# Optimization experiments

Measured on AMD Instinct MI355X. Metric: run time of the kernel, lower is better.

## Reference

```python
import jax, jax.numpy as jnp
import numpy as np

JITTER = 0.05  # posterior-covariance jitter (constructor arg `jitter`)
TWO_PI = 2.0 * np.pi


def _local_k(x1, x2, ls, std):
    # 1-D RBF kernel: x1 (A,), x2 (B,) -> (A, B)
    d2 = jnp.square(x1[:, None] - x2[None, :])
    return (std * std) * jnp.exp(-0.5 * d2 / (ls * ls))


def setup_inputs() -> dict:
    key = jax.random.key(0)
    ks = jax.random.split(key, 8)
    N, D, M = 3072, 4, 512
    X = jax.random.normal(ks[0], (N, D), dtype=jnp.float32)
    y = jax.random.normal(ks[1], (N, 1), dtype=jnp.float32)
    X_bar = jax.random.normal(ks[2], (M, D), dtype=jnp.float32)
    # learned parameters (moderate positive values so fp32 Choleskys are stable)
    local_gp_ls = 1.0 + 0.1 * jax.random.normal(ks[3], (D,), dtype=jnp.float32)
    local_gp_std = 0.5 + 0.05 * jax.random.normal(ks[4], (D,), dtype=jnp.float32)
    local_gp_noise_std = 0.3 * jnp.ones((D,), dtype=jnp.float32)
    local_ls = 0.3 + 0.5 * jax.random.uniform(ks[5], (M, D), dtype=jnp.float32)
    global_gp_std = jnp.array([0.7], dtype=jnp.float32)
    global_gp_noise_std = jnp.array([0.5], dtype=jnp.float32)
    return {
        "X": X, "y": y, "X_bar": X_bar,
        "local_gp_ls": local_gp_ls, "local_gp_std": local_gp_std,
        "local_gp_noise_std": local_gp_noise_std, "local_ls": local_ls,
        "global_gp_std": global_gp_std, "global_gp_noise_std": global_gp_noise_std,
    }


def reference(X, y, X_bar, local_gp_ls, local_gp_std, local_gp_noise_std,
              local_ls, global_gp_std, global_gp_noise_std):
    # NSGP.nlml() in training mode.
    N, D = X.shape
    M = X_bar.shape[0]
    dtype = X.dtype
    eyeM = jnp.eye(M, dtype=dtype)
    eyeN = jnp.eye(N, dtype=dtype)
    log_lbar = jnp.log(jnp.abs(local_ls))  # (M, D)

    def per_dim(xb, xd, ls, std, noise, loglb):
        # local GP over inducing points for one input dimension
        k = _local_k(xb, xb, ls, std) + (noise * noise) * eyeM  # (M, M)
        c = jnp.linalg.cholesky(k)
        alpha = jax.scipy.linalg.cho_solve((c, True), loglb[:, None])  # (M, 1)
        kstar = _local_k(xd, xb, ls, std)  # (N, M)
        l = jnp.exp(kstar @ alpha)[:, 0]   # (N,) predicted lengthscales
        kss = _local_k(xd, xd, ls, std)    # (N, N)
        v = jax.scipy.linalg.cho_solve((c, True), kstar.T)  # (M, N)
        kpost = kss - kstar @ v + JITTER * eyeN             # posterior cov
        pc = jnp.linalg.cholesky(kpost)
        Bd = jnp.sum(jnp.log(jnp.diagonal(pc)))
        return l, Bd

    # batch the per-dimension local-GP work across the D input dims
    l_dn, B_d = jax.vmap(per_dim, in_axes=(1, 1, 0, 0, 0, 1))(
        X_bar, X, local_gp_ls, local_gp_std, local_gp_noise_std, log_lbar)
    l = l_dn.T  # (N, D)

    # nonstationary global kernel (Gibbs kernel)
    l1 = l[:, None, :]                    # (N, 1, D)
    l2 = l[None, :, :]                    # (1, N, D)
    lsq = l1 * l1 + l2 * l2               # (N, N, D)
    suffix = jnp.prod(jnp.sqrt(2.0 * l1 * l2 / lsq), axis=2)  # (N, N)
    d2 = jnp.square(X[:, None, :] - X[None, :, :])            # (N, N, D)
    gvar = global_gp_std[0] * global_gp_std[0]
    K = gvar * suffix * jnp.exp(-jnp.sum(d2 / lsq, axis=2))
    K = K + (global_gp_noise_std[0] ** 2) * eyeN

    L = jnp.linalg.cholesky(K)
    alpha = jax.scipy.linalg.cho_solve((L, True), y)  # (N, 1)
    log2pi = jnp.log(jnp.asarray(TWO_PI, dtype))
    A = 0.5 * ((y.T @ alpha)[0, 0]
               + jnp.sum(jnp.log(jnp.diagonal(L)))
               + N * log2pi)
    B = jnp.sum(B_d) + 0.5 * (M * D * log2pi)
    return A + B
```

## Files before the change

kernel.cpp:

```cpp
#include <hip/hip_runtime.h>
#include <math.h>

#define N_   3072
#define D_   4
#define M_   512
#define NPAD 3200
#define NB   128
#define PW   32
#define NBLK (NPAD/NB)
#define MBLK (M_/NB)
#define JITTER_ 0.05f
#define CBORD 32768.0f
#define LTS  132

__device__ void syrk64(float* A, int lda, int gr0, int gc0, int k0, int valid,
                       float* As, float* Bs, int lt) {
  const int tx = lt & 15, ty = lt >> 4;
  float acc[4][4];
  #pragma unroll
  for (int i=0;i<4;++i){acc[i][0]=0.f;acc[i][1]=0.f;acc[i][2]=0.f;acc[i][3]=0.f;}
  for (int ks = 0; ks < NB; ks += 32) {
    __syncthreads();
    if (valid) {
      for (int t = lt; t < 64*8; t += 256) {
        int rr = t >> 3, qq = t & 7;
        float4 v = *(const float4*)&A[(size_t)(gr0+rr)*lda + k0 + ks + qq*4];
        As[(qq*4+0)*68+rr]=v.x; As[(qq*4+1)*68+rr]=v.y;
        As[(qq*4+2)*68+rr]=v.z; As[(qq*4+3)*68+rr]=v.w;
        float4 w = *(const float4*)&A[(size_t)(gc0+rr)*lda + k0 + ks + qq*4];
        Bs[(qq*4+0)*68+rr]=w.x; Bs[(qq*4+1)*68+rr]=w.y;
        Bs[(qq*4+2)*68+rr]=w.z; Bs[(qq*4+3)*68+rr]=w.w;
      }
    }
    __syncthreads();
    if (valid) {
      #pragma unroll
      for (int kk = 0; kk < 32; ++kk) {
        float a[4], b[4];
        *(float4*)a = *(const float4*)&As[kk*68 + ty*4];
        *(float4*)b = *(const float4*)&Bs[kk*68 + tx*4];
        #pragma unroll
        for (int i=0;i<4;++i)
          #pragma unroll
          for (int u=0;u<4;++u) acc[i][u] += a[i]*b[u];
      }
    }
  }
  if (valid) {
    #pragma unroll
    for (int i=0;i<4;++i) {
      size_t off = (size_t)(gr0 + ty*4 + i)*lda + gc0 + tx*4;
      float4 v = *(const float4*)&A[off];
      v.x -= acc[i][0]; v.y -= acc[i][1]; v.z -= acc[i][2]; v.w -= acc[i][3];
      *(float4*)&A[off] = v;
    }
  }
}

__device__ void presub64(const float* A, int lda, int j0, int p0, int sr, int sc,
                         int valid, float* As, float* Bs, float* LT_, int lt) {
  const int tx = lt & 15, ty = lt >> 4;
  float acc[4][4];
  #pragma unroll
  for (int i=0;i<4;++i){acc[i][0]=0.f;acc[i][1]=0.f;acc[i][2]=0.f;acc[i][3]=0.f;}
  for (int ks = 0; ks < NB; ks += 32) {
    __syncthreads();
    if (valid) {
      for (int t = lt; t < 64*8; t += 256) {
        int rr = t >> 3, qq = t & 7;
        float4 v = *(const float4*)&A[(size_t)(j0+sr*64+rr)*lda + p0 + ks + qq*4];
        As[(qq*4+0)*68+rr]=v.x; As[(qq*4+1)*68+rr]=v.y;
        As[(qq*4+2)*68+rr]=v.z; As[(qq*4+3)*68+rr]=v.w;
        float4 w = *(const float4*)&A[(size_t)(j0+sc*64+rr)*lda + p0 + ks + qq*4];
        Bs[(qq*4+0)*68+rr]=w.x; Bs[(qq*4+1)*68+rr]=w.y;
        Bs[(qq*4+2)*68+rr]=w.z; Bs[(qq*4+3)*68+rr]=w.w;
      }
    }
    __syncthreads();
    if (valid) {
      #pragma unroll
      for (int kk = 0; kk < 32; ++kk) {
        float a[4], b[4];
        *(float4*)a = *(const float4*)&As[kk*68 + ty*4];
        *(float4*)b = *(const float4*)&Bs[kk*68 + tx*4];
        #pragma unroll
        for (int i=0;i<4;++i)
          #pragma unroll
          for (int u=0;u<4;++u) acc[i][u] += a[i]*b[u];
      }
    }
  }
  if (valid) {
    #pragma unroll
    for (int i=0;i<4;++i)
      #pragma unroll
      for (int u=0;u<4;++u) {
        int rr = sr*64 + ty*4 + i, cc = sc*64 + tx*4 + u;
        if (cc <= rr) LT_[cc*LTS + rr] -= acc[i][u];
      }
  }
}

__device__ void potrf_duty(float* A, int lda, int b, int presub, int doInv,
                           float* Tinv, float* logsum, int slot, int limit,
                           float* LT_, float* SM_, float* pivd_) {
  const int tid = threadIdx.x;
  const int j0 = b * NB;
  for (int t = tid; t < NB*NB; t += 512) {
    int r = t >> 7, c = t & 127;
    float v = 0.f;
    if (c <= r) v = A[(size_t)(j0+r)*lda + (j0+c)];
    LT_[c*LTS + r] = v;
  }
  if (presub) {
    int half = tid >> 8, lt = tid & 255;
    float* As = SM_ + half*4352; float* Bs = As + 2176;
    const int p0 = j0 - NB;
    presub64(A, lda, j0, p0, half, 0, 1, As, Bs, LT_, lt);
    presub64(A, lda, j0, p0, 1, 1, half==0 ? 1 : 0, As, Bs, LT_, lt);
  }
  __syncthreads();
  #pragma unroll
  for (int p = 0; p < 4; ++p) {
    const int pc0 = p*PW, pc1 = pc0 + PW;
    for (int j = pc0; j < pc1; ++j) {
      float dd = fmaxf(LT_[j*LTS + j], 1e-30f);
      if (tid == 0) pivd_[j] = dd;
      float rd = 1.0f / dd;
      int wn = pc1 - 1 - j;
      for (int t = tid; t < wn*NB; t += 512) {
        int c = j + 1 + (t >> 7);
        int i = t & 127;
        if (i >= c) LT_[c*LTS + i] -= LT_[j*LTS + i] * LT_[j*LTS + c] * rd;
      }
      __syncthreads();
    }
    for (int t = tid; t < PW*NB; t += 512) {
      int jc = pc0 + (t >> 7);
      int i  = t & 127;
      float dd = pivd_[jc];
      if (i > jc)       LT_[jc*LTS + i] *= rsqrtf(dd);
      else if (i == jc) LT_[jc*LTS + i] = sqrtf(dd);
    }
    __syncthreads();
    if (pc1 < NB) {
      const int rem = NB - pc1, g4 = rem >> 2;
      for (int t = tid; t < g4*g4; t += 512) {
        int tr = t / g4, tc = t - tr*g4;
        if (tc > tr) continue;
        int i0 = pc1 + tr*4, c0 = pc1 + tc*4;
        float acc2[4][4];
        #pragma unroll
        for (int i=0;i<4;++i){acc2[i][0]=0.f;acc2[i][1]=0.f;acc2[i][2]=0.f;acc2[i][3]=0.f;}
        #pragma unroll
        for (int jj = 0; jj < PW; ++jj) {
          float av[4], bv[4];
          *(float4*)av = *(const float4*)&LT_[(pc0+jj)*LTS + i0];
          *(float4*)bv = *(const float4*)&LT_[(pc0+jj)*LTS + c0];
          #pragma unroll
          for (int i=0;i<4;++i)
            #pragma unroll
            for (int u=0;u<4;++u) acc2[i][u] += av[i]*bv[u];
        }
        #pragma unroll
        for (int i=0;i<4;++i)
          #pragma unroll
          for (int u=0;u<4;++u) {
            int rr = i0+i, cc = c0+u;
            if (cc <= rr) LT_[cc*LTS + rr] -= acc2[i][u];
          }
      }
      __syncthreads();
    }
  }
  for (int t = tid; t < NB*NB; t += 512) {
    int r = t >> 7, c = t & 127;
    if (c <= r) A[(size_t)(j0+r)*lda + (j0+c)] = LT_[c*LTS + r];
  }
  {
    float lg = 0.f;
    if (tid < NB) {
      int g = j0 + tid;
      if (g < limit) lg = 0.5f * logf(pivd_[tid]);
    }
    for (int o = 32; o; o >>= 1) lg += __shfl_down(lg, o);
    int wv = tid >> 6;
    if ((tid & 63) == 0 && wv < 2) logsum[slot*2 + wv] = lg;
  }
  if (!doInv) return;
  float* Wp = SM_;
  float* Tt = SM_ + 10240;
  for (int t = tid; t < 4*1024; t += 512) {
    int I = t >> 10, e = t & 1023;
    int r = e >> 5, c = e & 31;
    Wp[(I*(I+1)/2 + I)*1024 + e] = (r == c) ? 1.f : 0.f;
  }
  __syncthreads();
  {
    int wI = tid >> 7;
    int lane = tid & 127;
    float* Rb = &Wp[(wI*(wI+1)/2 + wI)*1024];
    for (int j = 0; j < 32; ++j) {
      float dinv = 1.0f / LT_[(wI*32+j)*LTS + (wI*32+j)];
      for (int t = lane; t < 1024; t += 128) {
        int i = t >> 5, c = t & 31;
        if (i > j && c <= j)
          Rb[i*32 + c] -= LT_[(wI*32+j)*LTS + (wI*32+i)] * Rb[j*32 + c] * dinv;
      }
      __syncthreads();
    }
    for (int t = lane; t < 1024; t += 128) {
      int i = t >> 5, c = t & 31;
      if (c <= i) Rb[i*32 + c] *= 1.0f / LT_[(wI*32+i)*LTS + (wI*32+i)];
    }
    __syncthreads();
  }
  #pragma unroll
  for (int dist = 1; dist < 4; ++dist) {
    const int nb = 4 - dist;
    for (int t = tid; t < nb*1024; t += 512) {
      int bb = t >> 10, e = t & 1023;
      int r = e >> 5, c = e & 31;
      int J = bb, I = bb + dist;
      float s = 0.f;
      for (int K = J; K < I; ++K) {
        const float* Wkj = &Wp[(K*(K+1)/2 + J)*1024];
        #pragma unroll
        for (int k = 0; k < 32; ++k)
          s += LT_[(K*32+k)*LTS + (I*32+r)] * Wkj[k*32 + c];
      }
      Tt[bb*1024 + e] = s;
    }
    __syncthreads();
    for (int t = tid; t < nb*1024; t += 512) {
      int bb = t >> 10, e = t & 1023;
      int r = e >> 5, c = e & 31;
      int J = bb, I = bb + dist;
      const float* Wii = &Wp[(I*(I+1)/2 + I)*1024];
      float s = 0.f;
      #pragma unroll
      for (int k = 0; k < 32; ++k)
        s += Wii[r*32 + k] * Tt[bb*1024 + k*32 + c];
      Wp[(I*(I+1)/2 + J)*1024 + e] = -s;
    }
    __syncthreads();
  }
  for (int t = tid; t < NB*32; t += 512) {
    int i = t >> 5, c4 = (t & 31) * 4;
    int I = i >> 5, J = c4 >> 5;
    float4 v;
    if (J <= I) {
      const float* Wij = &Wp[(I*(I+1)/2 + J)*1024 + (i & 31)*32 + (c4 & 31)];
      v = *(const float4*)Wij;
    } else v = make_float4(0.f, 0.f, 0.f, 0.f);
    *(float4*)&Tinv[i*NB + c4] = v;
  }
}

__global__ __launch_bounds__(512, 1)
void k_step(float* Abase, size_t aStride, int lda, int bpot, int presub, int doInv,
            float* TinvBase, size_t tStrideZ, size_t tStrideK,
            float* logsum, int slotBase, int limit,
            int R0, int q, int k0) {
  __shared__ __align__(16) float LT[128*LTS];
  __shared__ __align__(16) float SM[13312];
  __shared__ float pivd[NB];
  const int z = blockIdx.z;
  float* A = Abase + (size_t)z*aStride;

  if (blockIdx.x == 0) {
    potrf_duty(A, lda, bpot, presub, doInv,
               TinvBase + (size_t)z*tStrideZ + (size_t)bpot*tStrideK,
               logsum, slotBase + z*32 + bpot, limit, LT, SM, pivd);
    return;
  }
  const int tid = threadIdx.x;
  int half = tid >> 8, lt = tid & 255;
  int tileIdx = (blockIdx.x - 1)*2 + half;
  int ntiles = q*(q+1)/2 - 3;
  int valid = (tileIdx < ntiles) ? 1 : 0;
  int idxp = valid ? tileIdx + 3 : 3;
  int r = (int)((sqrtf(8.f*(float)idxp + 1.f) - 1.f)*0.5f);
  while ((r+1)*(r+2)/2 <= idxp) ++r;
  while (r*(r+1)/2 > idxp) --r;
  int c = idxp - r*(r+1)/2;
  syrk64(A, lda, (R0+r)*64, (R0+c)*64, k0, valid,
         SM + half*4352, SM + half*4352 + 2176, lt);
}

__global__ __launch_bounds__(256)
void k_trsm(float* Abase, size_t aStride, int lda, int kblk,
            const float* TinvBase, size_t tStride) {
  __shared__ float As[32*68];
  __shared__ float Ts[32*132];
  const int tid = threadIdx.x;
  float* A = Abase + (size_t)blockIdx.z * aStride;
  const float* Tinv = TinvBase + (size_t)blockIdx.z * tStride;
  const int k0 = kblk * NB;
  const int row0 = k0 + NB + blockIdx.x * 64;
  const int tx = tid & 15, ty = tid >> 4;
  float acc[4][8];
  #pragma unroll
  for (int i = 0; i < 4; ++i)
    #pragma unroll
    for (int u = 0; u < 8; ++u) acc[i][u] = 0.f;
  for (int ks = 0; ks < NB; ks += 32) {
    for (int t = tid; t < 64*8; t += 256) {
      int r = t >> 3, q = t & 7;
      float4 v = *(const float4*)&A[(size_t)(row0 + r)*lda + k0 + ks + q*4];
      As[(q*4+0)*68 + r] = v.x; As[(q*4+1)*68 + r] = v.y;
      As[(q*4+2)*68 + r] = v.z; As[(q*4+3)*68 + r] = v.w;
    }
    for (int t = tid; t < 128*8; t += 256) {
      int c = t >> 3, q = t & 7;
      float4 v = *(const float4*)&Tinv[c*NB + ks + q*4];
      Ts[(q*4+0)*132 + c] = v.x; Ts[(q*4+1)*132 + c] = v.y;
      Ts[(q*4+2)*132 + c] = v.z; Ts[(q*4+3)*132 + c] = v.w;
    }
    __syncthreads();
    #pragma unroll
    for (int kk = 0; kk < 32; ++kk) {
      float a[4], b[8];
      *(float4*)a      = *(const float4*)&As[kk*68 + ty*4];
      *(float4*)&b[0]  = *(const float4*)&Ts[kk*132 + tx*8];
      *(float4*)&b[4]  = *(const float4*)&Ts[kk*132 + tx*8 + 4];
      #pragma unroll
      for (int i = 0; i < 4; ++i)
        #pragma unroll
        for (int u = 0; u < 8; ++u) acc[i][u] += a[i]*b[u];
    }
    __syncthreads();
  }
  #pragma unroll
  for (int i = 0; i < 4; ++i) {
    int r = row0 + ty*4 + i;
    *(float4*)&A[(size_t)r*lda + k0 + tx*8]     = make_float4(acc[i][0],acc[i][1],acc[i][2],acc[i][3]);
    *(float4*)&A[(size_t)r*lda + k0 + tx*8 + 4] = make_float4(acc[i][4],acc[i][5],acc[i][6],acc[i][7]);
  }
}

__global__ __launch_bounds__(256)
void k_build_kb(const float* Xbar, const float* lsp, const float* stdp, const float* noisep,
                float* KbBase, size_t kbStride, int dimBase) {
  int z = blockIdx.z, d = dimBase + z;
  float* Kb = KbBase + (size_t)z*kbStride;
  int idx = blockIdx.x*256 + threadIdx.x;
  if (idx >= M_*M_) return;
  int i = idx >> 9, j = idx & 511;
  float ls = lsp[d], sd = stdp[d], nz = noisep[d];
  float df = Xbar[i*D_ + d] - Xbar[j*D_ + d];
  float v = sd*sd*expf(-0.5f*df*df/(ls*ls));
  if (i == j) v += nz*nz;
  Kb[idx] = v;
}

__global__ __launch_bounds__(256)
void k_build_kstar(const float* X, const float* Xbar, const float* lsp, const float* stdp,
                   float* KSBase, size_t ksStride, int dimBase) {
  int z = blockIdx.z, d = dimBase + z;
  float* KS = KSBase + (size_t)z*ksStride;
  int idx = blockIdx.x*256 + threadIdx.x;
  if (idx >= N_*M_) return;
  int i = idx >> 9, j = idx & 511;
  float ls = lsp[d], sd = stdp[d];
  float df = X[i*D_ + d] - Xbar[j*D_ + d];
  KS[idx] = sd*sd*expf(-0.5f*df*df/(ls*ls));
}

__global__ __launch_bounds__(256)
void k_csolve(float* CBase, size_t cStride, const float* KbBase, size_t kbStride,
              const float* TinvKbBase, size_t tkbStride, int J) {
  __shared__ float sm[12672];
  const int tid = threadIdx.x;
  float* C = CBase + (size_t)blockIdx.z*cStride;
  const float* L = KbBase + (size_t)blockIdx.z*kbStride;
  const float* Tinv = TinvKbBase + (size_t)blockIdx.z*tkbStride + (size_t)J*NB*NB;
  const int row0 = blockIdx.x*64;
  const int tx = tid & 15, ty = tid >> 4;
  float* As = sm; float* Ls = sm + 2176;
  float* Xs = sm; float* Ts = sm + 8448;
  float acc[4][8];
  #pragma unroll
  for (int i=0;i<4;++i) {
    const float* p = &C[(size_t)(row0+ty*4+i)*M_ + J*NB + tx*8];
    float4 v0 = *(const float4*)p, v1 = *(const float4*)(p+4);
    acc[i][0]=v0.x; acc[i][1]=v0.y; acc[i][2]=v0.z; acc[i][3]=v0.w;
    acc[i][4]=v1.x; acc[i][5]=v1.y; acc[i][6]=v1.z; acc[i][7]=v1.w;
  }
  for (int P = 0; P < J; ++P) {
    for (int ks = 0; ks < NB; ks += 32) {
// ... 182 lines not shown
__global__ __launch_bounds__(256)
void k_kfinal(const float* X, const float* lvec, const float* y,
              const float* gstd, const float* gnoise, float* A) {
  int idx = blockIdx.x*256 + threadIdx.x;
  if (idx >= NPAD*NPAD) return;
  int gi = idx / NPAD, gj = idx - (idx/NPAD)*NPAD;
  float v;
  if (gi < N_ && gj < N_) {
    float gv = gstd[0]*gstd[0];
    float prod = 1.f, s = 0.f;
    #pragma unroll
    for (int d = 0; d < D_; ++d) {
      float l1 = lvec[gi*D_ + d], l2 = lvec[gj*D_ + d];
      float lsq = l1*l1 + l2*l2;
      prod *= 2.f*l1*l2/lsq;
      float df = X[gi*D_ + d] - X[gj*D_ + d];
      s += df*df/lsq;
    }
    v = gv * sqrtf(prod) * expf(-s);
    if (gi == gj) v += gnoise[0]*gnoise[0];
  } else if (gi == N_ && gj < N_) v = y[gj];
  else if (gj == N_ && gi < N_) v = y[gi];
  else if (gi == N_ && gj == N_) v = CBORD;
  else v = (gi == gj) ? 1.f : 0.f;
  A[idx] = v;
}

__global__ void k_finalize(const float* A, const float* logsum, float* out) {
  if (threadIdx.x != 0 || blockIdx.x != 0) return;
  float sumB = 0.f;
  for (int z = 0; z < 4; ++z)
    for (int k = 0; k < NBLK; ++k) {
      int slot = z*32 + k;
      sumB += logsum[slot*2] + logsum[slot*2+1];
    }
  float sumL = 0.f;
  for (int k = 0; k < NBLK; ++k) {
    int slot = 128 + k;
    sumL += logsum[slot*2] + logsum[slot*2+1];
  }
  float lb = A[(size_t)N_*NPAD + N_];
  float yKy = CBORD - lb*lb;
  const float LOG2PI = 1.8378770664093453f;
  float Aterm = 0.5f*(yKy + sumL + (float)N_*LOG2PI);
  float Bterm = sumB + 0.5f*(float)(M_*D_)*LOG2PI;
  out[0] = Aterm + Bterm;
}

static void run_chain(float* A, size_t aS, int lda, int nblk,
                      float* Tinv, size_t tz, size_t tk, int invAll,
                      float* lgs, int slotBase, int limit, int nz,
                      hipStream_t stream) {
  int doInv0 = (invAll || nblk > 1) ? 1 : 0;
  k_step<<<dim3(1,1,nz),512,0,stream>>>(A,aS,lda, 0,0,doInv0, Tinv,tz,tk,
                                        lgs,slotBase,limit, 0,0,0);
  for (int k = 0; k < nblk-1; ++k) {
    int m = nblk-1-k;
    k_trsm<<<dim3(2*m,1,nz),256,0,stream>>>(A,aS,lda,k, Tinv + (size_t)k*tk, tz);
    int q2 = 2*m, ntiles = q2*(q2+1)/2 - 3;
    int nbx = 1 + (ntiles+1)/2;
    int doInv = (invAll || (k+1 < nblk-1)) ? 1 : 0;
    k_step<<<dim3(nbx,1,nz),512,0,stream>>>(A,aS,lda, k+1,1,doInv, Tinv,tz,tk,
                                            lgs,slotBase,limit, (k+1)*2, q2, k*NB);
  }
}

extern "C" void kernel_launch(void* const* d_in, const int* in_sizes, int n_in,
                              void* d_out, int out_size, void* d_ws, size_t ws_size,
                              hipStream_t stream) {
  const float* X    = (const float*)d_in[0];
  const float* y    = (const float*)d_in[1];
  const float* Xbar = (const float*)d_in[2];
  const float* lgls = (const float*)d_in[3];
  const float* lgstd= (const float*)d_in[4];
  const float* lgnz = (const float*)d_in[5];
  const float* lls  = (const float*)d_in[6];
  const float* gstd = (const float*)d_in[7];
  const float* gnz  = (const float*)d_in[8];
  float* out = (float*)d_out;

  const size_t A_SZ   = (size_t)NPAD*NPAD;
  const size_t KS_SZ  = (size_t)N_*M_;
  const size_t KB_SZ  = (size_t)M_*M_;
  const size_t TKB_SZ = (size_t)4*NB*NB;
  const size_t TBG_SZ = (size_t)NB*NB;
  const size_t W_SZ   = (size_t)M_;
  const size_t LV_SZ  = (size_t)N_*D_;
  const size_t LOG_SZ = 1024;

  size_t need2 = (5*A_SZ + 4*(KS_SZ + KB_SZ + TKB_SZ + W_SZ) + 5*TBG_SZ
                  + LV_SZ + LOG_SZ + 1024);
  size_t per1  = A_SZ + KS_SZ + KB_SZ + TKB_SZ + TBG_SZ + W_SZ;
  size_t need1 = 4*per1 + LV_SZ + LOG_SZ + 256;

  if (ws_size >= need2 * sizeof(float)) {
    float* p = (float*)d_ws;
    float* A    = p; p += 5*A_SZ;
    float* KS   = p; p += 4*KS_SZ;
    float* Kb   = p; p += 4*KB_SZ;
    float* Tkb  = p; p += 4*TKB_SZ;
    float* Tbig = p; p += 5*TBG_SZ;
    float* wv   = p; p += 4*W_SZ;
    float* lv   = p; p += LV_SZ;
    float* lgs  = p; p += LOG_SZ;

    k_build_kb<<<dim3((M_*M_+255)/256,1,4),256,0,stream>>>(Xbar,lgls,lgstd,lgnz,Kb,KB_SZ,0);
    run_chain(Kb, KB_SZ, M_, MBLK, Tkb, TKB_SZ, (size_t)NB*NB, 1, lgs, 192, 0, 4, stream);
    k_fwdsub<<<dim3(1,1,4),256,0,stream>>>(Kb,KB_SZ,Tkb,TKB_SZ,lls,wv,W_SZ,0);
    k_build_kstar<<<dim3((N_*M_+255)/256,1,4),256,0,stream>>>(X,Xbar,lgls,lgstd,KS,KS_SZ,0);
    for (int J = 0; J < MBLK; ++J)
      k_csolve<<<dim3(N_/64,1,4),256,0,stream>>>(KS,KS_SZ,Kb,KB_SZ,Tkb,TKB_SZ,J);
    k_gemv_l<<<dim3(N_/4,1,4),256,0,stream>>>(KS,KS_SZ,wv,W_SZ,lv,0);
    k_kpost<<<dim3(NPAD/64,NPAD/64,4),256,0,stream>>>(X,lgls,lgstd,KS,KS_SZ,A,A_SZ,0);
    k_kfinal<<<dim3((NPAD*NPAD+255)/256,1,1),256,0,stream>>>(X,lv,y,gstd,gnz,A+4*A_SZ);
    run_chain(A, A_SZ, NPAD, NBLK, Tbig, TBG_SZ, 0, 0, lgs, 0, N_, 5, stream);
    k_finalize<<<1,64,0,stream>>>(A+4*A_SZ,lgs,out);
    return;
  }

  bool batched = ws_size >= need1 * sizeof(float);
  int nz = batched ? 4 : 1;
  float* p = (float*)d_ws;
  float* A    = p; p += (size_t)nz*A_SZ;
  float* KS   = p; p += (size_t)nz*KS_SZ;
  float* Kb   = p; p += (size_t)nz*KB_SZ;
  float* Tkb  = p; p += (size_t)nz*TKB_SZ;
  float* Tbig = p; p += (size_t)nz*TBG_SZ;
  float* wv   = p; p += (size_t)nz*W_SZ;
  float* lv   = p; p += LV_SZ;
  float* lgs  = p; p += LOG_SZ;

  int npass = batched ? 1 : 4;
  for (int pass = 0; pass < npass; ++pass) {
    int dimBase  = batched ? 0 : pass;
    int slotBase = batched ? 0 : pass*32;
    k_build_kb<<<dim3((M_*M_+255)/256,1,nz),256,0,stream>>>(Xbar,lgls,lgstd,lgnz,Kb,KB_SZ,dimBase);
    run_chain(Kb, KB_SZ, M_, MBLK, Tkb, TKB_SZ, (size_t)NB*NB, 1, lgs, 192+slotBase, 0, nz, stream);
    k_fwdsub<<<dim3(1,1,nz),256,0,stream>>>(Kb,KB_SZ,Tkb,TKB_SZ,lls,wv,W_SZ,dimBase);
    k_build_kstar<<<dim3((N_*M_+255)/256,1,nz),256,0,stream>>>(X,Xbar,lgls,lgstd,KS,KS_SZ,dimBase);
    for (int J = 0; J < MBLK; ++J)
      k_csolve<<<dim3(N_/64,1,nz),256,0,stream>>>(KS,KS_SZ,Kb,KB_SZ,Tkb,TKB_SZ,J);
    k_gemv_l<<<dim3(N_/4,1,nz),256,0,stream>>>(KS,KS_SZ,wv,W_SZ,lv,dimBase);
    k_kpost<<<dim3(NPAD/64,NPAD/64,nz),256,0,stream>>>(X,lgls,lgstd,KS,KS_SZ,A,A_SZ,dimBase);
    run_chain(A, A_SZ, NPAD, NBLK, Tbig, TBG_SZ, 0, 0, lgs, slotBase, N_, nz, stream);
  }
  k_kfinal<<<dim3((NPAD*NPAD+255)/256,1,1),256,0,stream>>>(X,lv,y,gstd,gnz,A);
  run_chain(A, A_SZ, NPAD, NBLK, Tbig, TBG_SZ, 0, 0, lgs, 128, N_, 1, stream);
  k_finalize<<<1,64,0,stream>>>(A,lgs,out);
}
```

Baseline: 8.000 ms.

## Fuse panel TRSM with next diagonal POTRF and run SYRK as separate full-grid kernel

Reorganizes the blocked Cholesky schedule. The panel TRSM is now merged with the next block's POTRF in one kernel: block 0 solves the first two 64-row tiles and then factors the next diagonal block, while the other blocks solve the remaining tiles. The trailing SYRK update moves to its own kernel over a 2D tile grid that skips the upper triangle and the already-updated diagonal tiles. Tinv storage grows to one slot per block column so a stored inverse is not overwritten while it is still being read. The trade-off is a serial panel step still gated by one block, plus a 2D SYRK launch where roughly half the blocks exit at once.

```diff
diff --git a/kernel.cpp b/kernel.cpp
--- a/kernel.cpp
+++ b/kernel.cpp
@@ -13,47 +13,46 @@
 #define CBORD 32768.0f
 #define LTS  132
 
-__device__ void syrk64(float* A, int lda, int gr0, int gc0, int k0, int valid,
-                       float* As, float* Bs, int lt) {
+__device__ void trsm_tile64(float* A, int lda, int row0, int k0, const float* Tinv,
+                            float* As, float* Ts, int lt) {
   const int tx = lt & 15, ty = lt >> 4;
-  float acc[4][4];
-  #pragma unroll
-  for (int i=0;i<4;++i){acc[i][0]=0.f;acc[i][1]=0.f;acc[i][2]=0.f;acc[i][3]=0.f;}
+  float acc[4][8];
+  #pragma unroll
+  for (int i = 0; i < 4; ++i)
+    #pragma unroll
+    for (int u = 0; u < 8; ++u) acc[i][u] = 0.f;
   for (int ks = 0; ks < NB; ks += 32) {
-    __syncthreads();
-    if (valid) {
-      for (int t = lt; t < 64*8; t += 256) {
-        int rr = t >> 3, qq = t & 7;
-        float4 v = *(const float4*)&A[(size_t)(gr0+rr)*lda + k0 + ks + qq*4];
-        As[(qq*4+0)*68+rr]=v.x; As[(qq*4+1)*68+rr]=v.y;
-        As[(qq*4+2)*68+rr]=v.z; As[(qq*4+3)*68+rr]=v.w;
-        float4 w = *(const float4*)&A[(size_t)(gc0+rr)*lda + k0 + ks + qq*4];
-        Bs[(qq*4+0)*68+rr]=w.x; Bs[(qq*4+1)*68+rr]=w.y;
-        Bs[(qq*4+2)*68+rr]=w.z; Bs[(qq*4+3)*68+rr]=w.w;
-      }
-    }
-    __syncthreads();
-    if (valid) {
+    for (int t = lt; t < 64*8; t += 256) {
+      int r = t >> 3, q = t & 7;
+      float4 v = *(const float4*)&A[(size_t)(row0 + r)*lda + k0 + ks + q*4];
+      As[(q*4+0)*68 + r] = v.x; As[(q*4+1)*68 + r] = v.y;
+      As[(q*4+2)*68 + r] = v.z; As[(q*4+3)*68 + r] = v.w;
+    }
+    for (int t = lt; t < 128*8; t += 256) {
+      int c = t >> 3, q = t & 7;
+      float4 v = *(const float4*)&Tinv[c*NB + ks + q*4];
+      Ts[(q*4+0)*132 + c] = v.x; Ts[(q*4+1)*132 + c] = v.y;
+      Ts[(q*4+2)*132 + c] = v.z; Ts[(q*4+3)*132 + c] = v.w;
+    }
+    __syncthreads();
+    #pragma unroll
+    for (int kk = 0; kk < 32; ++kk) {
+      float a[4], b[8];
+      *(float4*)a      = *(const float4*)&As[kk*68 + ty*4];
+      *(float4*)&b[0]  = *(const float4*)&Ts[kk*132 + tx*8];
+      *(float4*)&b[4]  = *(const float4*)&Ts[kk*132 + tx*8 + 4];
       #pragma unroll
-      for (int kk = 0; kk < 32; ++kk) {
-        float a[4], b[4];
-        *(float4*)a = *(const float4*)&As[kk*68 + ty*4];
-        *(float4*)b = *(const float4*)&Bs[kk*68 + tx*4];
-        #pragma unroll
-        for (int i=0;i<4;++i)
-          #pragma unroll
-          for (int u=0;u<4;++u) acc[i][u] += a[i]*b[u];
-      }
-    }
-  }
-  if (valid) {
-    #pragma unroll
-    for (int i=0;i<4;++i) {
-      size_t off = (size_t)(gr0 + ty*4 + i)*lda + gc0 + tx*4;
-      float4 v = *(const float4*)&A[off];
-      v.x -= acc[i][0]; v.y -= acc[i][1]; v.z -= acc[i][2]; v.w -= acc[i][3];
-      *(float4*)&A[off] = v;
-    }
+      for (int i = 0; i < 4; ++i)
+        #pragma unroll
+        for (int u = 0; u < 8; ++u) acc[i][u] += a[i]*b[u];
+    }
+    __syncthreads();
+  }
+  #pragma unroll
+  for (int i = 0; i < 4; ++i) {
+    size_t off = (size_t)(row0 + ty*4 + i)*lda + k0 + tx*8;
+    *(float4*)&A[off]     = make_float4(acc[i][0],acc[i][1],acc[i][2],acc[i][3]);
+    *(float4*)&A[off + 4] = make_float4(acc[i][4],acc[i][5],acc[i][6],acc[i][7]);
   }
 }
 
@@ -258,84 +257,85 @@
 }
 
 __global__ __launch_bounds__(512, 1)
-void k_step(float* Abase, size_t aStride, int lda, int bpot, int presub, int doInv,
-            float* TinvBase, size_t tStrideZ, size_t tStrideK,
-            float* logsum, int slotBase, int limit,
-            int R0, int q, int k0) {
+void k_panel(float* Abase, size_t aStride, int lda, int k, int init, int doInv,
+             float* TinvBase, size_t tz, size_t tk,
+             float* logsum, int slotBase, int limit, int nblk) {
   __shared__ __align__(16) float LT[128*LTS];
   __shared__ __align__(16) float SM[13312];
   __shared__ float pivd[NB];
   const int z = blockIdx.z;
   float* A = Abase + (size_t)z*aStride;
+  float* Tz = TinvBase + (size_t)z*tz;
+  const int tid = threadIdx.x;
+
+  if (init) {
+    if (blockIdx.x == 0)
+      potrf_duty(A, lda, 0, 0, doInv, Tz, logsum, slotBase + z*32, limit,
+                 LT, SM, pivd);
+    return;
+  }
+  const int m = nblk - 1 - k;
+  const float* TinvK = Tz + (size_t)k*tk;
+  int half = tid >> 8, lt = tid & 255;
+  float* As = SM + half*6400;
+  float* Ts = As + 2176;
 
   if (blockIdx.x == 0) {
-    potrf_duty(A, lda, bpot, presub, doInv,
-               TinvBase + (size_t)z*tStrideZ + (size_t)bpot*tStrideK,
-               logsum, slotBase + z*32 + bpot, limit, LT, SM, pivd);
-    return;
-  }
-  const int tid = threadIdx.x;
-  int half = tid >> 8, lt = tid & 255;
-  int tileIdx = (blockIdx.x - 1)*2 + half;
-  int ntiles = q*(q+1)/2 - 3;
-  int valid = (tileIdx < ntiles) ? 1 : 0;
-  int idxp = valid ? tileIdx + 3 : 3;
-  int r = (int)((sqrtf(8.f*(float)idxp + 1.f) - 1.f)*0.5f);
-  while ((r+1)*(r+2)/2 <= idxp) ++r;
-  while (r*(r+1)/2 > idxp) --r;
-  int c = idxp - r*(r+1)/2;
-  syrk64(A, lda, (R0+r)*64, (R0+c)*64, k0, valid,
-         SM + half*4352, SM + half*4352 + 2176, lt);
+    trsm_tile64(A, lda, (k+1)*NB + half*64, k*NB, TinvK, As, Ts, lt);
+    __syncthreads();
+    potrf_duty(A, lda, k+1, 1, doInv, Tz + (size_t)(k+1)*tk,
+               logsum, slotBase + z*32 + (k+1), limit, LT, SM, pivd);
+  } else {
+    int t = 2 + (blockIdx.x - 1)*2 + half;
+    if (t < 2*m)
+      trsm_tile64(A, lda, (k+1)*NB + t*64, k*NB, TinvK, As, Ts, lt);
+  }
 }
 
 __global__ __launch_bounds__(256)
-void k_trsm(float* Abase, size_t aStride, int lda, int kblk,
-            const float* TinvBase, size_t tStride) {
+void k_syrk(float* Abase, size_t aStride, int lda, int kblk) {
+  if (blockIdx.y > blockIdx.x) return;
+  if (blockIdx.x < 2 && blockIdx.y < 2) return;
   __shared__ float As[32*68];
-  __shared__ float Ts[32*132];
+  __shared__ float Bs[32*68];
   const int tid = threadIdx.x;
   float* A = Abase + (size_t)blockIdx.z * aStride;
-  const float* Tinv = TinvBase + (size_t)blockIdx.z * tStride;
   const int k0 = kblk * NB;
   const int row0 = k0 + NB + blockIdx.x * 64;
+  const int col0 = k0 + NB + blockIdx.y * 64;
   const int tx = tid & 15, ty = tid >> 4;
-  float acc[4][8];
-  #pragma unroll
-  for (int i = 0; i < 4; ++i)
-    #pragma unroll
-    for (int u = 0; u < 8; ++u) acc[i][u] = 0.f;
+  float acc[4][4];
+  #pragma unroll
+  for (int i=0;i<4;++i) { acc[i][0]=0.f;acc[i][1]=0.f;acc[i][2]=0.f;acc[i][3]=0.f; }
   for (int ks = 0; ks < NB; ks += 32) {
     for (int t = tid; t < 64*8; t += 256) {
       int r = t >> 3, q = t & 7;
       float4 v = *(const float4*)&A[(size_t)(row0 + r)*lda + k0 + ks + q*4];
       As[(q*4+0)*68 + r] = v.x; As[(q*4+1)*68 + r] = v.y;
       As[(q*4+2)*68 + r] = v.z; As[(q*4+3)*68 + r] = v.w;
-    }
-    for (int t = tid; t < 128*8; t += 256) {
-      int c = t >> 3, q = t & 7;
-      float4 v = *(const float4*)&Tinv[c*NB + ks + q*4];
-      Ts[(q*4+0)*132 + c] = v.x; Ts[(q*4+1)*132 + c] = v.y;
-      Ts[(q*4+2)*132 + c] = v.z; Ts[(q*4+3)*132 + c] = v.w;
+      float4 w = *(const float4*)&A[(size_t)(col0 + r)*lda + k0 + ks + q*4];
+      Bs[(q*4+0)*68 + r] = w.x; Bs[(q*4+1)*68 + r] = w.y;
+      Bs[(q*4+2)*68 + r] = w.z; Bs[(q*4+3)*68 + r] = w.w;
     }
     __syncthreads();
     #pragma unroll
     for (int kk = 0; kk < 32; ++kk) {
-      float a[4], b[8];
-      *(float4*)a      = *(const float4*)&As[kk*68 + ty*4];
-      *(float4*)&b[0]  = *(const float4*)&Ts[kk*132 + tx*8];
-      *(float4*)&b[4]  = *(const float4*)&Ts[kk*132 + tx*8 + 4];
+      float a[4], b[4];
+      *(float4*)a = *(const float4*)&As[kk*68 + ty*4];
+      *(float4*)b = *(const float4*)&Bs[kk*68 + tx*4];
       #pragma unroll
-      for (int i = 0; i < 4; ++i)
-        #pragma unroll
-        for (int u = 0; u < 8; ++u) acc[i][u] += a[i]*b[u];
-    }
-    __syncthreads();
-  }
-  #pragma unroll
-  for (int i = 0; i < 4; ++i) {
-    int r = row0 + ty*4 + i;
-    *(float4*)&A[(size_t)r*lda + k0 + tx*8]     = make_float4(acc[i][0],acc[i][1],acc[i][2],acc[i][3]);
-    *(float4*)&A[(size_t)r*lda + k0 + tx*8 + 4] = make_float4(acc[i][4],acc[i][5],acc[i][6],acc[i][7]);
+      for (int i=0;i<4;++i)
+        #pragma unroll
+        for (int u=0;u<4;++u) acc[i][u] += a[i]*b[u];
+    }
+    __syncthreads();
+  }
+  #pragma unroll
+  for (int i=0;i<4;++i) {
+    size_t off = (size_t)(row0 + ty*4 + i)*lda + col0 + tx*4;
+    float4 v = *(const float4*)&A[off];
+    v.x -= acc[i][0]; v.y -= acc[i][1]; v.z -= acc[i][2]; v.w -= acc[i][3];
+    *(float4*)&A[off] = v;
   }
 }
 
@@ -624,16 +624,15 @@
                       float* lgs, int slotBase, int limit, int nz,
                       hipStream_t stream) {
   int doInv0 = (invAll || nblk > 1) ? 1 : 0;
-  k_step<<<dim3(1,1,nz),512,0,stream>>>(A,aS,lda, 0,0,doInv0, Tinv,tz,tk,
-                                        lgs,slotBase,limit, 0,0,0);
+  k_panel<<<dim3(1,1,nz),512,0,stream>>>(A,aS,lda, 0,1,doInv0, Tinv,tz,tk,
+                                         lgs,slotBase,limit, nblk);
   for (int k = 0; k < nblk-1; ++k) {
     int m = nblk-1-k;
-    k_trsm<<<dim3(2*m,1,nz),256,0,stream>>>(A,aS,lda,k, Tinv + (size_t)k*tk, tz);
-    int q2 = 2*m, ntiles = q2*(q2+1)/2 - 3;
-    int nbx = 1 + (ntiles+1)/2;
     int doInv = (invAll || (k+1 < nblk-1)) ? 1 : 0;
-    k_step<<<dim3(nbx,1,nz),512,0,stream>>>(A,aS,lda, k+1,1,doInv, Tinv,tz,tk,
-                                            lgs,slotBase,limit, (k+1)*2, q2, k*NB);
+    k_panel<<<dim3(m,1,nz),512,0,stream>>>(A,aS,lda, k,0,doInv, Tinv,tz,tk,
+                                           lgs,slotBase,limit, nblk);
+    if (m >= 2)
+      k_syrk<<<dim3(2*m,2*m,nz),256,0,stream>>>(A,aS,lda,k);
   }
 }
 
@@ -654,8 +653,8 @@
   const size_t A_SZ   = (size_t)NPAD*NPAD;
   const size_t KS_SZ  = (size_t)N_*M_;
   const size_t KB_SZ  = (size_t)M_*M_;
-  const size_t TKB_SZ = (size_t)4*NB*NB;
-  const size_t TBG_SZ = (size_t)NB*NB;
+  const size_t TKB_SZ = (size_t)MBLK*NB*NB;
+  const size_t TBG_SZ = (size_t)NBLK*NB*NB;
   const size_t W_SZ   = (size_t)M_;
   const size_t LV_SZ  = (size_t)N_*D_;
   const size_t LOG_SZ = 1024;
@@ -685,7 +684,7 @@
     k_gemv_l<<<dim3(N_/4,1,4),256,0,stream>>>(KS,KS_SZ,wv,W_SZ,lv,0);
     k_kpost<<<dim3(NPAD/64,NPAD/64,4),256,0,stream>>>(X,lgls,lgstd,KS,KS_SZ,A,A_SZ,0);
     k_kfinal<<<dim3((NPAD*NPAD+255)/256,1,1),256,0,stream>>>(X,lv,y,gstd,gnz,A+4*A_SZ);
-    run_chain(A, A_SZ, NPAD, NBLK, Tbig, TBG_SZ, 0, 0, lgs, 0, N_, 5, stream);
+    run_chain(A, A_SZ, NPAD, NBLK, Tbig, TBG_SZ, (size_t)NB*NB, 0, lgs, 0, N_, 5, stream);
     k_finalize<<<1,64,0,stream>>>(A+4*A_SZ,lgs,out);
     return;
   }
@@ -714,9 +713,9 @@
       k_csolve<<<dim3(N_/64,1,nz),256,0,stream>>>(KS,KS_SZ,Kb,KB_SZ,Tkb,TKB_SZ,J);
     k_gemv_l<<<dim3(N_/4,1,nz),256,0,stream>>>(KS,KS_SZ,wv,W_SZ,lv,dimBase);
     k_kpost<<<dim3(NPAD/64,NPAD/64,nz),256,0,stream>>>(X,lgls,lgstd,KS,KS_SZ,A,A_SZ,dimBase);
-    run_chain(A, A_SZ, NPAD, NBLK, Tbig, TBG_SZ, 0, 0, lgs, slotBase, N_, nz, stream);
+    run_chain(A, A_SZ, NPAD, NBLK, Tbig, TBG_SZ, (size_t)NB*NB, 0, lgs, slotBase, N_, nz, stream);
   }
   k_kfinal<<<dim3((NPAD*NPAD+255)/256,1,1),256,0,stream>>>(X,lv,y,gstd,gnz,A);
-  run_chain(A, A_SZ, NPAD, NBLK, Tbig, TBG_SZ, 0, 0, lgs, 128, N_, 1, stream);
+  run_chain(A, A_SZ, NPAD, NBLK, Tbig, TBG_SZ, (size_t)NB*NB, 0, lgs, 128, N_, 1, stream);
   k_finalize<<<1,64,0,stream>>>(A,lgs,out);
 }
```

Measured after the change: 8.684 ms. +8.5%, slower.

## Split panel Cholesky into two 64-column halves to shrink shared memory

Applied to the files above, without the earlier changes.

The diagonal-block factorization no longer holds a full 128x128 tile in LDS. It factors the left 64-column panel, then updates and factors the trailing 64x64 block separately, and builds the triangular inverse from two 64x64 inverses plus an off-diagonal product. The smaller LDS footprint lets launch bounds rise from 1 to 4 blocks per CU, so the syrk tile blocks that run alongside get more occupancy. In exchange, the trailing-block work reads global memory directly in several places, including the presub dot products and the second inverse, which could slow the serial critical-path block.

```diff
diff --git a/kernel.cpp b/kernel.cpp
--- a/kernel.cpp
+++ b/kernel.cpp
@@ -6,12 +6,10 @@
 #define M_   512
 #define NPAD 3200
 #define NB   128
-#define PW   32
 #define NBLK (NPAD/NB)
 #define MBLK (M_/NB)
 #define JITTER_ 0.05f
 #define CBORD 32768.0f
-#define LTS  132
 
 __device__ void syrk64(float* A, int lda, int gr0, int gc0, int k0, int valid,
                        float* As, float* Bs, int lt) {
@@ -57,106 +55,90 @@
   }
 }
 
-__device__ void presub64(const float* A, int lda, int j0, int p0, int sr, int sc,
-                         int valid, float* As, float* Bs, float* LT_, int lt) {
-  const int tx = lt & 15, ty = lt >> 4;
-  float acc[4][4];
-  #pragma unroll
-  for (int i=0;i<4;++i){acc[i][0]=0.f;acc[i][1]=0.f;acc[i][2]=0.f;acc[i][3]=0.f;}
-  for (int ks = 0; ks < NB; ks += 32) {
-    __syncthreads();
-    if (valid) {
-      for (int t = lt; t < 64*8; t += 256) {
-        int rr = t >> 3, qq = t & 7;
-        float4 v = *(const float4*)&A[(size_t)(j0+sr*64+rr)*lda + p0 + ks + qq*4];
-        As[(qq*4+0)*68+rr]=v.x; As[(qq*4+1)*68+rr]=v.y;
-        As[(qq*4+2)*68+rr]=v.z; As[(qq*4+3)*68+rr]=v.w;
-        float4 w = *(const float4*)&A[(size_t)(j0+sc*64+rr)*lda + p0 + ks + qq*4];
-        Bs[(qq*4+0)*68+rr]=w.x; Bs[(qq*4+1)*68+rr]=w.y;
-        Bs[(qq*4+2)*68+rr]=w.z; Bs[(qq*4+3)*68+rr]=w.w;
-      }
-    }
-    __syncthreads();
-    if (valid) {
-      #pragma unroll
-      for (int kk = 0; kk < 32; ++kk) {
-        float a[4], b[4];
-        *(float4*)a = *(const float4*)&As[kk*68 + ty*4];
-        *(float4*)b = *(const float4*)&Bs[kk*68 + tx*4];
-        #pragma unroll
-        for (int i=0;i<4;++i)
+__device__ void panel_duty(float* A, int lda, int bpot, int presub, int doInv,
+                           float* Tinv, float* logsum, int slot, int limit,
+                           float* SM, float* pivd) {
+  const int tid = threadIdx.x;
+  const int dj = bpot * NB;
+  float* LP = SM;
+  for (int t = tid; t < 64*NB; t += 512) {
+    int r = t >> 6, c = t & 63;
+    LP[c*132 + r] = (c <= r) ? A[(size_t)(dj+r)*lda + dj + c] : 0.f;
+  }
+  if (presub) {
+    const int p0 = dj - NB;
+    float* As = SM + 8448; float* Bs = As + 2176;
+    const int tx = tid & 15, ty = tid >> 4;
+    for (int sr = 0; sr < 2; ++sr) {
+      float acc[2][4];
+      #pragma unroll
+      for (int i=0;i<2;++i){acc[i][0]=0.f;acc[i][1]=0.f;acc[i][2]=0.f;acc[i][3]=0.f;}
+      for (int ks = 0; ks < NB; ks += 32) {
+        __syncthreads();
+        for (int t = tid; t < 64*8; t += 512) {
+          int rr = t >> 3, qq = t & 7;
+          float4 v = *(const float4*)&A[(size_t)(dj+sr*64+rr)*lda + p0 + ks + qq*4];
+          As[(qq*4+0)*68+rr]=v.x; As[(qq*4+1)*68+rr]=v.y;
+          As[(qq*4+2)*68+rr]=v.z; As[(qq*4+3)*68+rr]=v.w;
+          float4 w = *(const float4*)&A[(size_t)(dj+rr)*lda + p0 + ks + qq*4];
+          Bs[(qq*4+0)*68+rr]=w.x; Bs[(qq*4+1)*68+rr]=w.y;
+          Bs[(qq*4+2)*68+rr]=w.z; Bs[(qq*4+3)*68+rr]=w.w;
+        }
+        __syncthreads();
+        #pragma unroll
+        for (int kk = 0; kk < 32; ++kk) {
+          float a0 = As[kk*68 + ty*2], a1 = As[kk*68 + ty*2 + 1];
+          float b[4];
+          *(float4*)b = *(const float4*)&Bs[kk*68 + tx*4];
           #pragma unroll
-          for (int u=0;u<4;++u) acc[i][u] += a[i]*b[u];
-      }
-    }
-  }
-  if (valid) {
-    #pragma unroll
-    for (int i=0;i<4;++i)
-      #pragma unroll
-      for (int u=0;u<4;++u) {
-        int rr = sr*64 + ty*4 + i, cc = sc*64 + tx*4 + u;
-        if (cc <= rr) LT_[cc*LTS + rr] -= acc[i][u];
-      }
-  }
-}
-
-__device__ void potrf_duty(float* A, int lda, int b, int presub, int doInv,
-                           float* Tinv, float* logsum, int slot, int limit,
-                           float* LT_, float* SM_, float* pivd_) {
-  const int tid = threadIdx.x;
-  const int j0 = b * NB;
-  for (int t = tid; t < NB*NB; t += 512) {
-    int r = t >> 7, c = t & 127;
-    float v = 0.f;
-    if (c <= r) v = A[(size_t)(j0+r)*lda + (j0+c)];
-    LT_[c*LTS + r] = v;
-  }
-  if (presub) {
-    int half = tid >> 8, lt = tid & 255;
-    float* As = SM_ + half*4352; float* Bs = As + 2176;
-    const int p0 = j0 - NB;
-    presub64(A, lda, j0, p0, half, 0, 1, As, Bs, LT_, lt);
-    presub64(A, lda, j0, p0, 1, 1, half==0 ? 1 : 0, As, Bs, LT_, lt);
-  }
-  __syncthreads();
-  #pragma unroll
-  for (int p = 0; p < 4; ++p) {
-    const int pc0 = p*PW, pc1 = pc0 + PW;
+          for (int u=0;u<4;++u) { acc[0][u] += a0*b[u]; acc[1][u] += a1*b[u]; }
+        }
+      }
+      #pragma unroll
+      for (int i=0;i<2;++i)
+        #pragma unroll
+        for (int u=0;u<4;++u) {
+          int rr = sr*64 + ty*2 + i, cc = tx*4 + u;
+          if (cc <= rr) LP[cc*132 + rr] -= acc[i][u];
+        }
+    }
+  }
+  __syncthreads();
+  #pragma unroll
+  for (int p = 0; p < 2; ++p) {
+    const int pc0 = p*32, pc1 = pc0 + 32;
     for (int j = pc0; j < pc1; ++j) {
-      float dd = fmaxf(LT_[j*LTS + j], 1e-30f);
-      if (tid == 0) pivd_[j] = dd;
+      float dd = fmaxf(LP[j*132 + j], 1e-30f);
+      if (tid == 0) pivd[j] = dd;
       float rd = 1.0f / dd;
       int wn = pc1 - 1 - j;
       for (int t = tid; t < wn*NB; t += 512) {
         int c = j + 1 + (t >> 7);
         int i = t & 127;
-        if (i >= c) LT_[c*LTS + i] -= LT_[j*LTS + i] * LT_[j*LTS + c] * rd;
+        if (i >= c) LP[c*132 + i] -= LP[j*132 + i] * LP[j*132 + c] * rd;
       }
       __syncthreads();
     }
-    for (int t = tid; t < PW*NB; t += 512) {
-      int jc = pc0 + (t >> 7);
-      int i  = t & 127;
-      float dd = pivd_[jc];
-      if (i > jc)       LT_[jc*LTS + i] *= rsqrtf(dd);
-      else if (i == jc) LT_[jc*LTS + i] = sqrtf(dd);
-    }
-    __syncthreads();
-    if (pc1 < NB) {
-      const int rem = NB - pc1, g4 = rem >> 2;
-      for (int t = tid; t < g4*g4; t += 512) {
-        int tr = t / g4, tc = t - tr*g4;
-        if (tc > tr) continue;
-        int i0 = pc1 + tr*4, c0 = pc1 + tc*4;
+    for (int t = tid; t < 32*NB; t += 512) {
+      int jc = pc0 + (t >> 7), i = t & 127;
+      float dd = pivd[jc];
+      if (i > jc)       LP[jc*132 + i] *= rsqrtf(dd);
+      else if (i == jc) LP[jc*132 + i] = sqrtf(dd);
+    }
+    __syncthreads();
+    if (p == 0) {
+      for (int t = tid; t < 24*8; t += 512) {
+        int tr = t >> 3, tc = t & 7;
+        int i0 = 32 + tr*4, c0 = 32 + tc*4;
+        if (i0 + 3 < c0) continue;
         float acc2[4][4];
         #pragma unroll
         for (int i=0;i<4;++i){acc2[i][0]=0.f;acc2[i][1]=0.f;acc2[i][2]=0.f;acc2[i][3]=0.f;}
         #pragma unroll
-        for (int jj = 0; jj < PW; ++jj) {
+        for (int jj = 0; jj < 32; ++jj) {
           float av[4], bv[4];
-          *(float4*)av = *(const float4*)&LT_[(pc0+jj)*LTS + i0];
-          *(float4*)bv = *(const float4*)&LT_[(pc0+jj)*LTS + c0];
+          *(float4*)av = *(const float4*)&LP[jj*132 + i0];
+          *(float4*)bv = *(const float4*)&LP[jj*132 + c0];
           #pragma unroll
           for (int i=0;i<4;++i)
             #pragma unroll
@@ -167,116 +149,233 @@
           #pragma unroll
           for (int u=0;u<4;++u) {
             int rr = i0+i, cc = c0+u;
-            if (cc <= rr) LT_[cc*LTS + rr] -= acc2[i][u];
+            if (cc <= rr) LP[cc*132 + rr] -= acc2[i][u];
           }
       }
       __syncthreads();
     }
   }
-  for (int t = tid; t < NB*NB; t += 512) {
-    int r = t >> 7, c = t & 127;
-    if (c <= r) A[(size_t)(j0+r)*lda + (j0+c)] = LT_[c*LTS + r];
-  }
+  for (int t = tid; t < 64*NB; t += 512) {
+    int r = t >> 6, c = t & 63;
+    if (c <= r) A[(size_t)(dj+r)*lda + dj + c] = LP[c*132 + r];
+  }
+  __syncthreads();
+  float* DS = SM + 8448;
+  for (int t = tid; t < 64*64; t += 512) {
+    int r = t >> 6, c = t & 63;
+    DS[c*68 + r] = (c <= r) ? A[(size_t)(dj+64+r)*lda + dj+64 + c] : 0.f;
+  }
+  __syncthreads();
+  {
+    const int tx = tid & 15, ty = tid >> 4;
+    const int r0 = ty*2, c0 = tx*4;
+    float acc[2][4];
+    #pragma unroll
+    for (int i=0;i<2;++i){acc[i][0]=0.f;acc[i][1]=0.f;acc[i][2]=0.f;acc[i][3]=0.f;}
+    if (presub) {
+      const int p0 = dj - NB;
+      for (int kk = 0; kk < NB; kk += 4) {
+        float4 a0 = *(const float4*)&A[(size_t)(dj+64+r0)*lda + p0 + kk];
+        float4 a1 = *(const float4*)&A[(size_t)(dj+64+r0+1)*lda + p0 + kk];
+        #pragma unroll
+        for (int u=0;u<4;++u) {
+          float4 b = *(const float4*)&A[(size_t)(dj+64+c0+u)*lda + p0 + kk];
+          acc[0][u] += a0.x*b.x + a0.y*b.y + a0.z*b.z + a0.w*b.w;
+          acc[1][u] += a1.x*b.x + a1.y*b.y + a1.z*b.z + a1.w*b.w;
+        }
+      }
+    }
+    for (int kk = 0; kk < 64; ++kk) {
+      float a0 = LP[kk*132 + 64 + r0], a1 = LP[kk*132 + 64 + r0 + 1];
+      float b0 = LP[kk*132 + 64 + c0],     b1 = LP[kk*132 + 64 + c0 + 1];
+      float b2 = LP[kk*132 + 64 + c0 + 2], b3 = LP[kk*132 + 64 + c0 + 3];
+      acc[0][0]+=a0*b0; acc[0][1]+=a0*b1; acc[0][2]+=a0*b2; acc[0][3]+=a0*b3;
+      acc[1][0]+=a1*b0; acc[1][1]+=a1*b1; acc[1][2]+=a1*b2; acc[1][3]+=a1*b3;
+    }
+    #pragma unroll
+    for (int i=0;i<2;++i)
+      #pragma unroll
+      for (int u=0;u<4;++u) {
+        int rr = r0+i, cc = c0+u;
+        if (cc <= rr) DS[cc*68 + rr] -= acc[i][u];
+      }
+  }
+  __syncthreads();
+  #pragma unroll
+  for (int p = 0; p < 2; ++p) {
+    const int pc0 = p*32, pc1 = pc0 + 32;
+    for (int j = pc0; j < pc1; ++j) {
+      float dd = fmaxf(DS[j*68 + j], 1e-30f);
+      if (tid == 0) pivd[64 + j] = dd;
+      float rd = 1.0f / dd;
+      int wn = pc1 - 1 - j;
+      for (int t = tid; t < wn*64; t += 512) {
+        int c = j + 1 + (t >> 6);
+        int i = t & 63;
+        if (i >= c) DS[c*68 + i] -= DS[j*68 + i] * DS[j*68 + c] * rd;
+      }
+      __syncthreads();
+    }
+    for (int t = tid; t < 32*64; t += 512) {
+      int jc = pc0 + (t >> 6), i = t & 63;
+      float dd = pivd[64 + jc];
+      if (i > jc)       DS[jc*68 + i] *= rsqrtf(dd);
+      else if (i == jc) DS[jc*68 + i] = sqrtf(dd);
+    }
+    __syncthreads();
+    if (p == 0) {
+      for (int t = tid; t < 8*8; t += 512) {
+        int tr = t >> 3, tc = t & 7;
+        int i0 = 32 + tr*4, c0 = 32 + tc*4;
+        if (i0 + 3 < c0) continue;
+        float acc2[4][4];
+        #pragma unroll
+        for (int i=0;i<4;++i){acc2[i][0]=0.f;acc2[i][1]=0.f;acc2[i][2]=0.f;acc2[i][3]=0.f;}
+        #pragma unroll
+        for (int jj = 0; jj < 32; ++jj) {
+          float av[4], bv[4];
+          *(float4*)av = *(const float4*)&DS[jj*68 + i0];
+          *(float4*)bv = *(const float4*)&DS[jj*68 + c0];
+          #pragma unroll
+          for (int i=0;i<4;++i)
+            #pragma unroll
+            for (int u=0;u<4;++u) acc2[i][u] += av[i]*bv[u];
+        }
+        #pragma unroll
+        for (int i=0;i<4;++i)
+          #pragma unroll
+          for (int u=0;u<4;++u) {
+            int rr = i0+i, cc = c0+u;
+            if (cc <= rr) DS[cc*68 + rr] -= acc2[i][u];
+          }
+      }
+      __syncthreads();
+    }
+  }
+  for (int t = tid; t < 64*64; t += 512) {
+    int r = t >> 6, c = t & 63;
+    if (c <= r) A[(size_t)(dj+64+r)*lda + dj+64 + c] = DS[c*68 + r];
+  }
+  __syncthreads();
   {
     float lg = 0.f;
     if (tid < NB) {
-      int g = j0 + tid;
-      if (g < limit) lg = 0.5f * logf(pivd_[tid]);
+      int g = dj + tid;
+      if (g < limit) lg = 0.5f * logf(pivd[tid]);
     }
     for (int o = 32; o; o >>= 1) lg += __shfl_down(lg, o);
     int wv = tid >> 6;
     if ((tid & 63) == 0 && wv < 2) logsum[slot*2 + wv] = lg;
   }
   if (!doInv) return;
-  float* Wp = SM_;
-  float* Tt = SM_ + 10240;
-  for (int t = tid; t < 4*1024; t += 512) {
-    int I = t >> 10, e = t & 1023;
-    int r = e >> 5, c = e & 31;
-    Wp[(I*(I+1)/2 + I)*1024 + e] = (r == c) ? 1.f : 0.f;
+  float* R = SM + 8448;
+  for (int t = tid; t < 64*64; t += 512) {
+    int i = t >> 6, c = t & 63;
+    R[i*66 + c] = (i == c) ? 1.f : 0.f;
+  }
+  __syncthreads();
+  for (int j = 0; j < 64; ++j) {
+    float dinv = 1.0f / LP[j*132 + j];
+    int nc = j + 1, ni = 63 - j;
+    for (int t = tid; t < ni*nc; t += 512) {
+      int i = j + 1 + t / nc, c = t - (t / nc)*nc;
+      R[i*66 + c] -= LP[j*132 + i] * R[j*66 + c] * dinv;
+    }
+    __syncthreads();
+  }
+  for (int t = tid; t < 64*64; t += 512) {
+    int i = t >> 6, c = t & 63;
+    if (c <= i) R[i*66 + c] *= 1.0f / LP[i*132 + i];
+  }
+  __syncthreads();
+  for (int t = tid; t < 64*NB; t += 512) {
+    int i = t >> 7, c = t & 127;
+    Tinv[i*NB + c] = (c < 64) ? R[i*66 + c] : 0.f;
   }
   __syncthreads();
   {
-    int wI = tid >> 7;
-    int lane = tid & 127;
-    float* Rb = &Wp[(wI*(wI+1)/2 + wI)*1024];
-    for (int j = 0; j < 32; ++j) {
-      float dinv = 1.0f / LT_[(wI*32+j)*LTS + (wI*32+j)];
-      for (int t = lane; t < 1024; t += 128) {
-        int i = t >> 5, c = t & 31;
-        if (i > j && c <= j)
-          Rb[i*32 + c] -= LT_[(wI*32+j)*LTS + (wI*32+i)] * Rb[j*32 + c] * dinv;
-      }
-      __syncthreads();
-    }
-    for (int t = lane; t < 1024; t += 128) {
-      int i = t >> 5, c = t & 31;
-      if (c <= i) Rb[i*32 + c] *= 1.0f / LT_[(wI*32+i)*LTS + (wI*32+i)];
-    }
-    __syncthreads();
-  }
-  #pragma unroll
-  for (int dist = 1; dist < 4; ++dist) {
-    const int nb = 4 - dist;
-    for (int t = tid; t < nb*1024; t += 512) {
-      int bb = t >> 10, e = t & 1023;
-      int r = e >> 5, c = e & 31;
-      int J = bb, I = bb + dist;
-      float s = 0.f;
-      for (int K = J; K < I; ++K) {
-        const float* Wkj = &Wp[(K*(K+1)/2 + J)*1024];
-        #pragma unroll
-        for (int k = 0; k < 32; ++k)
-          s += LT_[(K*32+k)*LTS + (I*32+r)] * Wkj[k*32 + c];
-      }
-      Tt[bb*1024 + e] = s;
-    }
-    __syncthreads();
-    for (int t = tid; t < nb*1024; t += 512) {
-      int bb = t >> 10, e = t & 1023;
-      int r = e >> 5, c = e & 31;
-      int J = bb, I = bb + dist;
-      const float* Wii = &Wp[(I*(I+1)/2 + I)*1024];
-      float s = 0.f;
-      #pragma unroll
-      for (int k = 0; k < 32; ++k)
-        s += Wii[r*32 + k] * Tt[bb*1024 + k*32 + c];
-      Wp[(I*(I+1)/2 + J)*1024 + e] = -s;
-    }
-    __syncthreads();
-  }
-  for (int t = tid; t < NB*32; t += 512) {
-    int i = t >> 5, c4 = (t & 31) * 4;
-    int I = i >> 5, J = c4 >> 5;
-    float4 v;
-    if (J <= I) {
-      const float* Wij = &Wp[(I*(I+1)/2 + J)*1024 + (i & 31)*32 + (c4 & 31)];
-      v = *(const float4*)Wij;
-    } else v = make_float4(0.f, 0.f, 0.f, 0.f);
-    *(float4*)&Tinv[i*NB + c4] = v;
-  }
-}
-
-__global__ __launch_bounds__(512, 1)
+    const int tx = tid & 15, ty = tid >> 4;
+    const int r0 = ty*2, c0 = tx*4;
+    float acc[2][4];
+    #pragma unroll
+    for (int i=0;i<2;++i){acc[i][0]=0.f;acc[i][1]=0.f;acc[i][2]=0.f;acc[i][3]=0.f;}
+    for (int k = 0; k < 64; ++k) {
+      float a0 = LP[k*132 + 64 + r0], a1 = LP[k*132 + 64 + r0 + 1];
+      float4 b = *(const float4*)&Tinv[k*NB + c0];
+      acc[0][0]+=a0*b.x; acc[0][1]+=a0*b.y; acc[0][2]+=a0*b.z; acc[0][3]+=a0*b.w;
+      acc[1][0]+=a1*b.x; acc[1][1]+=a1*b.y; acc[1][2]+=a1*b.z; acc[1][3]+=a1*b.w;
+    }
+    __syncthreads();
+    #pragma unroll
+    for (int i=0;i<2;++i)
+      #pragma unroll
+      for (int u=0;u<4;++u) R[(r0+i)*66 + c0+u] = acc[i][u];
+  }
+  __syncthreads();
+  float* R2 = SM;
+  for (int t = tid; t < 64*64; t += 512) {
+    int i = t >> 6, c = t & 63;
+    R2[i*66 + c] = (i == c) ? 1.f : 0.f;
+  }
+  __syncthreads();
+  for (int j = 0; j < 64; ++j) {
+    float dinv = 1.0f / A[(size_t)(dj+64+j)*lda + dj+64 + j];
+    int nc = j + 1, ni = 63 - j;
+    for (int t = tid; t < ni*nc; t += 512) {
+      int i = j + 1 + t / nc, c = t - (t / nc)*nc;
+      R2[i*66 + c] -= A[(size_t)(dj+64+i)*lda + dj+64 + j] * R2[j*66 + c] * dinv;
+    }
+    __syncthreads();
+  }
+  for (int t = tid; t < 64*64; t += 512) {
+    int i = t >> 6, c = t & 63;
+    if (c <= i) R2[i*66 + c] *= 1.0f / A[(size_t)(dj+64+i)*lda + dj+64 + i];
+  }
+  __syncthreads();
+  {
+    const int tx = tid & 15, ty = tid >> 4;
+    const int r0 = ty*2, c0 = tx*4;
+    float acc[2][4];
+    #pragma unroll
+    for (int i=0;i<2;++i){acc[i][0]=0.f;acc[i][1]=0.f;acc[i][2]=0.f;acc[i][3]=0.f;}
+    for (int k = 0; k < 64; ++k) {
+      float a0 = R2[r0*66 + k], a1 = R2[(r0+1)*66 + k];
+      float b0 = R[k*66 + c0],     b1 = R[k*66 + c0 + 1];
+      float b2 = R[k*66 + c0 + 2], b3 = R[k*66 + c0 + 3];
+      acc[0][0]+=a0*b0; acc[0][1]+=a0*b1; acc[0][2]+=a0*b2; acc[0][3]+=a0*b3;
+      acc[1][0]+=a1*b0; acc[1][1]+=a1*b1; acc[1][2]+=a1*b2; acc[1][3]+=a1*b3;
+    }
+    #pragma unroll
+    for (int i=0;i<2;++i)
+      #pragma unroll
+      for (int u=0;u<4;++u)
+        Tinv[(size_t)(64 + r0 + i)*NB + c0 + u] = -acc[i][u];
+  }
+  for (int t = tid; t < 64*64; t += 512) {
+    int i = t >> 6, c = t & 63;
+    Tinv[(size_t)(64 + i)*NB + 64 + c] = R2[i*66 + c];
+  }
+}
+
+__global__ __launch_bounds__(512, 4)
 void k_step(float* Abase, size_t aStride, int lda, int bpot, int presub, int doInv,
             float* TinvBase, size_t tStrideZ, size_t tStrideK,
             float* logsum, int slotBase, int limit,
             int R0, int q, int k0) {
-  __shared__ __align__(16) float LT[128*LTS];
-  __shared__ __align__(16) float SM[13312];
+  __shared__ __align__(16) float SM[12800];
   __shared__ float pivd[NB];
   const int z = blockIdx.z;
   float* A = Abase + (size_t)z*aStride;
 
   if (blockIdx.x == 0) {
-    potrf_duty(A, lda, bpot, presub, doInv,
+    panel_duty(A, lda, bpot, presub, doInv,
                TinvBase + (size_t)z*tStrideZ + (size_t)bpot*tStrideK,
-               logsum, slotBase + z*32 + bpot, limit, LT, SM, pivd);
+               logsum, slotBase + z*32 + bpot, limit, SM, pivd);
     return;
   }
   const int tid = threadIdx.x;
-  int half = tid >> 8, lt = tid & 255;
-  int tileIdx = (blockIdx.x - 1)*2 + half;
+  int eng = tid >> 8, lt = tid & 255;
+  int tileIdx = (blockIdx.x - 1)*2 + eng;
   int ntiles = q*(q+1)/2 - 3;
   int valid = (tileIdx < ntiles) ? 1 : 0;
   int idxp = valid ? tileIdx + 3 : 3;
@@ -285,7 +384,7 @@
   while (r*(r+1)/2 > idxp) --r;
   int c = idxp - r*(r+1)/2;
   syrk64(A, lda, (R0+r)*64, (R0+c)*64, k0, valid,
-         SM + half*4352, SM + half*4352 + 2176, lt);
+         SM + eng*4352, SM + eng*4352 + 2176, lt);
 }
 
 __global__ __launch_bounds__(256)
```

After: 14.80 ms. +85.0%, slower.
